# Kernel tuning notes

Measured on AMD Instinct MI355X. Metric: run time of the kernel, lower is better.

The kernel has to match this reference:

```python
import jax, jax.numpy as jnp
import numpy as np

K = 3            # CRF kernel size
THETA0 = 0.5     # color bandwidth
THETA1 = 30.0    # spatial bandwidth
ALPHA0 = 3.0     # kernel scale
BASE = 0.45      # label clamping base
CRF_ITERS = 10   # mean-field iterations
NMS_SIGMA = 2.0  # gaussian matrix-NMS sigma


def _unfold(x, k=K):
    # torch.nn.Unfold(k, stride=1, padding=k//2): (B, C, H, W) -> (B, C, k*k, H*W)
    B, C, H, W = x.shape
    p = k // 2
    xp = jnp.pad(x, ((0, 0), (0, 0), (p, p), (p, p)))
    patches = jnp.stack([xp[:, :, i:i + H, j:j + W]
                         for i in range(k) for j in range(k)], axis=2)
    return patches.reshape(B, C, k * k, H * W)


def _matrix_nms(seg_masks, cate_labels, cate_scores, sigma=NMS_SIGMA):
    n = seg_masks.shape[0]
    m = seg_masks.reshape(n, -1).astype(jnp.float32)
    sum_m = m.sum(axis=1)                         # (n,)
    inter = m @ m.T                               # (n, n)
    union = sum_m[None, :] + sum_m[:, None] - inter
    triu = jnp.triu(jnp.ones((n, n), dtype=bool), k=1)
    iou = jnp.where(triu, inter / union, 0.0)
    label_eq = (cate_labels[None, :] == cate_labels[:, None]) & triu
    decay_iou = jnp.where(label_eq, iou, 0.0)
    comp = decay_iou.max(axis=0)                  # compensate IoU per candidate
    decay = jnp.exp(-sigma * decay_iou ** 2)
    compm = jnp.exp(-sigma * comp ** 2)[:, None]  # broadcast over columns (torch expand+T)
    coef = (decay / compm).min(axis=0)
    return cate_scores * coef


def _crf(feature_map, x, targets):
    B, C, H, W = feature_map.shape
    k2 = K * K
    # gaussian pairwise kernel from (shifted) color features
    fm = feature_map + 10.0
    uf = _unfold(fm)                              # (B, C, k2, H*W)
    idx = np.arange(k2)
    spatial = ((idx // K - K // 2) ** 2 + (idx % K - K // 2) ** 2).astype(np.float32)
    color = -((uf - fm.reshape(B, C, 1, H * W)) ** 2).sum(axis=1) / (2.0 * THETA0 ** 2)
    kernel = ALPHA0 * jnp.exp(color - jnp.asarray(spatial)[None, :, None] / (2.0 * THETA1 ** 2))
    kernel = kernel[:, None]                      # (B, 1, k2, H*W)

    # unary init
    xt = x * targets
    xt = (xt > 0.5).astype(jnp.float32) * (1.0 - 2.0 * BASE) + BASE
    ret = jnp.concatenate([1.0 - xt, xt], axis=1)  # (B, 2, H, W)
    ones_t = jnp.ones_like(targets)
    for _ in range(CRF_ITERS):
        uf_x = _unfold(-jnp.log(ret.reshape(2 * B, 1, H, W))).reshape(B, 2, k2, H * W)
        aggre = (uf_x * kernel).sum(axis=2)        # (B, 2, H*W)
        f = jnp.exp(-aggre).reshape(B, 2, H, W)
        f = f * jnp.concatenate([ones_t, targets], axis=1)  # gate fg channel by targets
        f = f + 1e-6
        f = f / f.sum(axis=1, keepdims=True)
        ret = (f > 0.5).astype(jnp.float32) * (1.0 - 2.0 * BASE) + BASE
    masks = (ret[:, 1:] > 0.5).astype(jnp.float32)  # (B, 1, H, W)
    count = masks.reshape(B, -1).sum(axis=1)
    valid = ((count >= H * W * 0.05) & (count <= H * W * 0.95)).astype(jnp.float32)
    return masks, valid


def setup_inputs() -> dict:
    key = jax.random.key(0)
    k1, k2, k3, k4, k5, k6 = jax.random.split(key, 6)
    n, h, w = 256, 128, 128
    ni, c = 64, 3
    seg_masks = (jax.random.uniform(k1, (n, h, w)) > 0.5).astype(jnp.float32)
    cate_scores = jnp.sort(jax.random.uniform(k2, (n,)))[::-1]
    feature_map = jax.random.uniform(k3, (ni, c, h, w))
    x = jax.random.uniform(k4, (ni, 1, h, w))
    targets = (jax.random.uniform(k5, (ni, 1, h, w)) > 0.3).astype(jnp.float32)
    cate_labels = jax.random.randint(k6, (n,), 0, 80, dtype=jnp.int64)
    return {"seg_masks": seg_masks, "cate_scores": cate_scores,
            "feature_map": feature_map, "x": x, "targets": targets,
            "cate_labels": cate_labels}


def reference(seg_masks, cate_scores, feature_map, x, targets, cate_labels):
    scores = _matrix_nms(seg_masks, cate_labels, cate_scores)
    masks, valid = _crf(feature_map, x, targets)
    return scores, masks, valid
```

## Files before the change

kernel.cpp:

```cpp
#include <hip/hip_runtime.h>
#include <stdint.h>

#define HW 16384
#define NI 64
#define NM 256
#define WORDS 256

#define PR 136
#define TROWS 32
#define WROWS 52
#define NTHREADS 832
#define NBLK 256
#define SR 34
#define SPR 27
#define SPSZ (SPR * PR)

#define OFF_PACKED (2u << 20)
#define OFF_DIOUT  0x280000u
#define OFF_COMPM  0x2C0000u
#define OFF_CNT    0x2C1000u

__device__ __forceinline__ unsigned long long spread4(unsigned long long t) {
    t &= 0xFFFFull;
    t = (t | (t << 24)) & 0x000000FF000000FFull;
    t = (t | (t << 12)) & 0x000F000F000F000Full;
    t = (t | (t << 6))  & 0x0303030303030303ull;
    t = (t | (t << 3))  & 0x1111111111111111ull;
    return t;
}

__device__ __forceinline__ void load_row(const float* __restrict__ fb,
                                         const int y, const int xc,
                                         float (&u)[3][4]) {
    #pragma clang fp contract(off)
    if ((unsigned)y < 128u) {
        const int pp = y * 128 + xc;
        float4 v0 = *(const float4*)&fb[pp];
        float4 v1 = *(const float4*)&fb[HW + pp];
        float4 v2 = *(const float4*)&fb[2 * HW + pp];
        u[0][0]=v0.x+10.0f; u[0][1]=v0.y+10.0f; u[0][2]=v0.z+10.0f; u[0][3]=v0.w+10.0f;
        u[1][0]=v1.x+10.0f; u[1][1]=v1.y+10.0f; u[1][2]=v1.z+10.0f; u[1][3]=v1.w+10.0f;
        u[2][0]=v2.x+10.0f; u[2][1]=v2.y+10.0f; u[2][2]=v2.z+10.0f; u[2][3]=v2.w+10.0f;
    } else {
        #pragma unroll
        for (int c = 0; c < 3; ++c)
            #pragma unroll
            for (int j = 0; j < 4; ++j) u[c][j] = 0.0f;
    }
}

__device__ __forceinline__ float cell_res(float n0, float n1, float n2,
                                          float c0, float c1, float c2,
                                          float sp) {
    #pragma clang fp contract(off)
    float d0 = n0 - c0, d1 = n1 - c1, d2 = n2 - c2;
    float ss = d0 * d0;
    ss = ss + d1 * d1;
    ss = ss + d2 * d2;
    float color = (-ss) / 0.5f;
    return 3.0f * expf(color - sp);
}

__device__ __forceinline__ void compute_row(
    const float (&uc)[3][4], const float (&ut)[3][4],
    const float (&lt)[3], const float (&rt)[3], const float (&lc)[3],
    const bool in_y, const bool in_t, const int q, float4 (&out)[4]) {
    #pragma clang fp contract(off)
    const float sp1 = 1.0f / 1800.0f;
    const float sp2 = 2.0f / 1800.0f;
    float r[4];
    r[0] = r[1] = r[2] = r[3] = 0.0f;
    if (in_y && in_t) {
        if (q > 0)
            r[0] = cell_res(lt[0], lt[1], lt[2], uc[0][0], uc[1][0], uc[2][0], sp2);
        r[1] = cell_res(ut[0][0], ut[1][0], ut[2][0], uc[0][1], uc[1][1], uc[2][1], sp2);
        r[2] = cell_res(ut[0][1], ut[1][1], ut[2][1], uc[0][2], uc[1][2], uc[2][2], sp2);
        r[3] = cell_res(ut[0][2], ut[1][2], ut[2][2], uc[0][3], uc[1][3], uc[2][3], sp2);
    }
    out[0] = make_float4(r[0], r[1], r[2], r[3]);
    r[0] = r[1] = r[2] = r[3] = 0.0f;
    if (in_y && in_t) {
        r[0] = cell_res(ut[0][0], ut[1][0], ut[2][0], uc[0][0], uc[1][0], uc[2][0], sp1);
        r[1] = cell_res(ut[0][1], ut[1][1], ut[2][1], uc[0][1], uc[1][1], uc[2][1], sp1);
        r[2] = cell_res(ut[0][2], ut[1][2], ut[2][2], uc[0][2], uc[1][2], uc[2][2], sp1);
        r[3] = cell_res(ut[0][3], ut[1][3], ut[2][3], uc[0][3], uc[1][3], uc[2][3], sp1);
    }
    out[1] = make_float4(r[0], r[1], r[2], r[3]);
    r[0] = r[1] = r[2] = r[3] = 0.0f;
    if (in_y && in_t) {
        r[0] = cell_res(ut[0][1], ut[1][1], ut[2][1], uc[0][0], uc[1][0], uc[2][0], sp2);
        r[1] = cell_res(ut[0][2], ut[1][2], ut[2][2], uc[0][1], uc[1][1], uc[2][1], sp2);
        r[2] = cell_res(ut[0][3], ut[1][3], ut[2][3], uc[0][2], uc[1][2], uc[2][2], sp2);
        if (q < 31)
            r[3] = cell_res(rt[0], rt[1], rt[2], uc[0][3], uc[1][3], uc[2][3], sp2);
    }
    out[2] = make_float4(r[0], r[1], r[2], r[3]);
    r[0] = r[1] = r[2] = r[3] = 0.0f;
    if (in_y) {
        if (q > 0)
            r[0] = cell_res(lc[0], lc[1], lc[2], uc[0][0], uc[1][0], uc[2][0], sp1);
        r[1] = cell_res(uc[0][0], uc[1][0], uc[2][0], uc[0][1], uc[1][1], uc[2][1], sp1);
        r[2] = cell_res(uc[0][1], uc[1][1], uc[2][1], uc[0][2], uc[1][2], uc[2][2], sp1);
        r[3] = cell_res(uc[0][2], uc[1][2], uc[2][2], uc[0][3], uc[1][3], uc[2][3], sp1);
    }
    out[3] = make_float4(r[0], r[1], r[2], r[3]);
}

__device__ __forceinline__ void stage_init_row(
    const float* __restrict__ x, const float* __restrict__ targets,
    uint32_t* __restrict__ stw0, uint32_t* __restrict__ stw1, const int img,
    const int y, const int wrow, const int q, const int xc, const bool inimg) {
    #pragma clang fp contract(off)
    uint32_t st = 0;
    if (inimg) {
        const size_t gp = (size_t)img * HW + y * 128 + xc;
        const float4 xv = *(const float4*)(x + gp);
        const float4 tv = *(const float4*)(targets + gp);
        float xs[4] = {xv.x, xv.y, xv.z, xv.w};
        float ts[4] = {tv.x, tv.y, tv.z, tv.w};
        #pragma unroll
        for (int j = 0; j < 4; ++j) {
            float xt = xs[j] * ts[j];
            int b1 = (xt > 0.5f) ? 1 : 0;
            int tb = (ts[j] > 0.5f) ? 1 : 0;
            st |= (uint32_t)(b1 | ((b1 ^ 1) << 1) | (tb << 2)) << (8 * j);
        }
    }
    stw0[wrow * SR + 1 + q] = st;
    if (!inimg) stw1[wrow * SR + 1 + q] = 0;
    if (q == 0)  { stw0[wrow * SR + 0]  = 0; stw1[wrow * SR + 0]  = 0; }
    if (q == 31) { stw0[wrow * SR + 33] = 0; stw1[wrow * SR + 33] = 0; }
}

__device__ __forceinline__ uint32_t crf_core(const float (&kw)[9][4],
                                             const uint32_t (&in9)[9]) {
    #pragma clang fp contract(off)
    const float l45 = 0.7985076962177716f;
    const float l55 = 0.5978370007556204f;
    const uint32_t wcen = in9[4];
    float lx1r[3][6], lx0r[3][6];
    #pragma unroll
    for (int r = 0; r < 3; ++r) {
        const uint32_t wm = in9[r * 3 + 0];
        const uint32_t wc = in9[r * 3 + 1];
        const uint32_t wp = in9[r * 3 + 2];
        unsigned char b[6];
        b[0] = wm >> 24;
        b[1] = wc & 0xff; b[2] = (wc >> 8) & 0xff;
        b[3] = (wc >> 16) & 0xff; b[4] = wc >> 24;
        b[5] = wp & 0xff;
        #pragma unroll
        for (int m = 0; m < 6; ++m) {
            lx1r[r][m] = (b[m] & 1) ? l55 : l45;
            lx0r[r][m] = (b[m] & 2) ? l55 : l45;
        }
    }
    float a0[4] = {0.f, 0.f, 0.f, 0.f}, a1[4] = {0.f, 0.f, 0.f, 0.f};
    #pragma unroll
    for (int k = 0; k < 9; ++k) {
        const int r = k / 3, m0 = k % 3;
        #pragma unroll
        for (int j = 0; j < 4; ++j) {
            const float kwv = kw[k][j];
            const float t1 = lx1r[r][j + m0] * kwv;
            const float t0 = lx0r[r][j + m0] * kwv;
            a1[j] = a1[j] + t1;
            a0[j] = a0[j] + t0;
        }
    }
    uint32_t ow = 0;
    #pragma unroll
    for (int j = 0; j < 4; ++j) {
        const unsigned char sc = (wcen >> (8 * j)) & 0xffu;
        const float tval = (sc & 4) ? 1.0f : 0.0f;
        const float e1 = expf(-a1[j]);
        const float e0 = expf(-a0[j]);
        const float m1 = e1 * tval;
        const float f1 = m1 + 1e-6f;
        const float f0 = e0 + 1e-6f;
        const float den = f0 + f1;
        const float r1 = f1 / den;
        const float r0v = f0 / den;
        const int s1 = (r1 > 0.5f) ? 1 : 0;
        const int s0 = (r0v > 0.5f) ? 1 : 0;
        ow |= (uint32_t)(s1 | (s0 << 1) | (sc & 4)) << (8 * j);
    }
    return ow;
}

__global__ __launch_bounds__(832, 4) void crf10_kernel(
    const float* __restrict__ feat, const float* __restrict__ seg,
    unsigned long long* __restrict__ packed, const float* __restrict__ x,
    const float* __restrict__ targets, float* __restrict__ out,
    int* __restrict__ counters) {
    #pragma clang fp contract(off)
    __shared__ float strip[3 * SPSZ];
    __shared__ uint32_t stw0[WROWS * SR];
    __shared__ uint32_t stw1[WROWS * SR];
    __shared__ int chg[10];

    const int tid = threadIdx.x, bid = blockIdx.x;
    const int img = bid >> 2;
    const int r0 = (bid & 3) * TROWS;
    const int relp = tid >> 5;
    const int q = tid & 31;
    const int xc = q * 4;
    const int wrowA = 2 * relp, wrowB = wrowA + 1;
    const int yA = r0 - 10 + wrowA, yB = yA + 1;
    const bool inA = (unsigned)yA < 128u, inB = (unsigned)yB < 128u;
    const int sbaseA = wrowA * SR + 1 + q, sbaseB = wrowB * SR + 1 + q;
    const float* fb = feat + (size_t)img * 3 * HW;

    {
        const int wave = tid >> 6, lane = tid & 63;
        const int gw = bid * 13 + wave;
        for (int gwi = gw; gwi < 16384; gwi += 3328) {
            const int i = gwi >> 6, w4 = gwi & 63;
            const float4 v =
                *(const float4*)&seg[(size_t)i * HW + w4 * 256 + lane * 4];
            unsigned long long b0 = __ballot(v.x > 0.5f);
            unsigned long long b1 = __ballot(v.y > 0.5f);
            unsigned long long b2 = __ballot(v.z > 0.5f);
            unsigned long long b3 = __ballot(v.w > 0.5f);
            if (lane < 4) {
                const int sh = lane * 16;
                unsigned long long word = spread4(b0 >> sh)
                                        | (spread4(b1 >> sh) << 1)
                                        | (spread4(b2 >> sh) << 2)
                                        | (spread4(b3 >> sh) << 3);
                packed[(size_t)(w4 * 4 + lane) * NM + i] = word;
            }
        }
    }

    float uT[3][4], uA[3][4], uB[3][4];
    load_row(fb, yA - 1, xc, uT);
    load_row(fb, yA, xc, uA);
    float lT[3], rT[3], lA[3], rA[3], lB[3];
    #pragma unroll
    for (int c = 0; c < 3; ++c) {
        lT[c] = __shfl_up(uT[c][3], 1);
        rT[c] = __shfl_down(uT[c][0], 1);
        lA[c] = __shfl_up(uA[c][3], 1);
        rA[c] = __shfl_down(uA[c][0], 1);
    }
    float4 ap[4], bp[4];
    compute_row(uA, uT, lT, rT, lA, inA, (unsigned)(yA - 1) < 128u, q, ap);
    load_row(fb, yB, xc, uB);
    #pragma unroll
    for (int c = 0; c < 3; ++c) lB[c] = __shfl_up(uB[c][3], 1);
    compute_row(uB, uA, lA, rA, lB, inB, inA, q, bp);

    #pragma unroll
    for (int k = 0; k < 3; ++k) {
        *(float4*)&strip[k * SPSZ + relp * PR + 4 + xc] = ap[k];
        if (q == 0)
            *(float4*)&strip[k * SPSZ + relp * PR + 0] = make_float4(0, 0, 0, 0);
        if (q == 31)
            *(float4*)&strip[k * SPSZ + relp * PR + 132] = make_float4(0, 0, 0, 0);
    }
    stage_init_row(x, targets, stw0, stw1, img, yA, wrowA, q, xc, inA);
    stage_init_row(x, targets, stw0, stw1, img, yB, wrowB, q, xc, inB);
    if (tid < 10) chg[tid] = 0;

    float a_s5 = __shfl_down(ap[3].x, 1); if (q == 31) a_s5 = 0.0f;
    float b_s5 = __shfl_down(bp[3].x, 1); if (q == 31) b_s5 = 0.0f;
    float b_s6 = __shfl_up(bp[2].w, 1);   if (q == 0)  b_s6 = 0.0f;
    float b_s8 = __shfl_down(bp[0].x, 1); if (q == 31) b_s8 = 0.0f;
    __syncthreads();

    const float kwA[9][4] = {
        {ap[0].x, ap[0].y, ap[0].z, ap[0].w},
        {ap[1].x, ap[1].y, ap[1].z, ap[1].w},
        {ap[2].x, ap[2].y, ap[2].z, ap[2].w},
        {ap[3].x, ap[3].y, ap[3].z, ap[3].w},
        {3.0f, 3.0f, 3.0f, 3.0f},
        {ap[3].y, ap[3].z, ap[3].w, a_s5},
        {b_s6, bp[2].x, bp[2].y, bp[2].z},
        {bp[1].x, bp[1].y, bp[1].z, bp[1].w},
        {bp[0].y, bp[0].z, bp[0].w, b_s8}};

    uint32_t pinA[9], pinB[9];
    uint32_t powvA = 0, powvB = 0;
    bool hpA = false, hpB = false;
    int cur = 0;
    for (int s = 0; s < 10; ++s) {
        const int lo = (r0 - 9 + s < 0) ? 0 : r0 - 9 + s;
        const int hi = (r0 + 41 - s > 128) ? 128 : r0 + 41 - s;
        const bool actA = (yA >= lo) && (yA < hi);
        const bool actB = (yB >= lo) && (yB < hi);
        const uint32_t* sw = cur ? stw1 : stw0;
        uint32_t* swn = cur ? stw0 : stw1;
        bool changed = false;
        if (actA || actB) {
            const uint32_t ra0 = sw[sbaseA - 1], ra1 = sw[sbaseA], ra2 = sw[sbaseA + 1];
            const uint32_t rb0 = sw[sbaseB - 1], rb1 = sw[sbaseB], rb2 = sw[sbaseB + 1];
            if (actA) {
                const uint32_t in9[9] = {sw[sbaseA - SR - 1], sw[sbaseA - SR],
                                         sw[sbaseA - SR + 1], ra0, ra1, ra2,
                                         rb0, rb1, rb2};
                bool same = hpA;
                #pragma unroll
                for (int m = 0; m < 9; ++m) same = same && (in9[m] == pinA[m]);
                uint32_t ow;
                if (same) {
                    ow = powvA;
                } else {
                    ow = crf_core(kwA, in9);
                    #pragma unroll
                    for (int m = 0; m < 9; ++m) pinA[m] = in9[m];
                    powvA = ow;
                    hpA = true;
                }
                swn[sbaseA] = ow;
                changed = (ow != ra1);
            }
            if (actB) {
                const uint32_t in9[9] = {ra0, ra1, ra2, rb0, rb1, rb2,
                                         sw[sbaseB + SR - 1], sw[sbaseB + SR],
                                         sw[sbaseB + SR + 1]};
                bool same = hpB;
                #pragma unroll
                for (int m = 0; m < 9; ++m) same = same && (in9[m] == pinB[m]);
                uint32_t ow;
                if (same) {
                    ow = powvB;
                } else {
                    const int cb = (relp + 1) * PR + 4 + xc;
                    const float4 c_p0 = *(const float4*)&strip[0 * SPSZ + cb];
                    const float4 c_p1 = *(const float4*)&strip[1 * SPSZ + cb];
                    const float4 c_p2 = *(const float4*)&strip[2 * SPSZ + cb];
                    const float  c_s6 = strip[2 * SPSZ + cb - 1];
                    const float  c_s8 = strip[0 * SPSZ + cb + 4];
                    const float kwB[9][4] = {
                        {bp[0].x, bp[0].y, bp[0].z, bp[0].w},
                        {bp[1].x, bp[1].y, bp[1].z, bp[1].w},
                        {bp[2].x, bp[2].y, bp[2].z, bp[2].w},
                        {bp[3].x, bp[3].y, bp[3].z, bp[3].w},
                        {3.0f, 3.0f, 3.0f, 3.0f},
                        {bp[3].y, bp[3].z, bp[3].w, b_s5},
                        {c_s6, c_p2.x, c_p2.y, c_p2.z},
                        {c_p1.x, c_p1.y, c_p1.z, c_p1.w},
                        {c_p0.y, c_p0.z, c_p0.w, c_s8}};
                    ow = crf_core(kwB, in9);
                    #pragma unroll
                    for (int m = 0; m < 9; ++m) pinB[m] = in9[m];
                    powvB = ow;
                    hpB = true;
                }
                swn[sbaseB] = ow;
                changed = changed || (ow != rb1);
            }
        }
        unsigned long long bal = __ballot(changed);
        if ((tid & 63) == 0 && bal) atomicOr(&chg[s], 1);
        __syncthreads();
        if (chg[s] == 0) break;
        cur ^= 1;
    }

    int cnt = 0;
    {
        const uint32_t* swf = cur ? stw1 : stw0;
        float* om = out + NM + (size_t)img * HW;
        if (yA >= r0 && yA < r0 + TROWS) {
            const uint32_t w = swf[sbaseA];
            *(float4*)(om + yA * 128 + xc) =
                make_float4((float)(w & 1), (float)((w >> 8) & 1),
                            (float)((w >> 16) & 1), (float)((w >> 24) & 1));
            cnt += __popc(w & 0x01010101u);
        }
        if (yB >= r0 && yB < r0 + TROWS) {
            const uint32_t w = swf[sbaseB];
            *(float4*)(om + yB * 128 + xc) =
                make_float4((float)(w & 1), (float)((w >> 8) & 1),
                            (float)((w >> 16) & 1), (float)((w >> 24) & 1));
            cnt += __popc(w & 0x01010101u);
        }
    }
    __syncthreads();
    {
        int* cred = (int*)strip;
        cred[tid] = cnt;
        if (tid < 192) cred[832 + tid] = 0;
        __syncthreads();
        for (int off = 512; off > 0; off >>= 1) {
            if (tid < off) cred[tid] += cred[tid + off];
            __syncthreads();
        }
        if (tid == 0) counters[bid] = cred[0];
    }
}

__global__ __launch_bounds__(256) void diou_compm_kernel(
    const unsigned long long* __restrict__ packed, const int* __restrict__ labels,
    float* __restrict__ diouT, float* __restrict__ compm) {
    #pragma clang fp contract(off)
    __shared__ unsigned long long colj[WORDS];
    __shared__ float red[NM];
    const int j = blockIdx.x, i = threadIdx.x;
    colj[i] = packed[i * NM + j];
    __syncthreads();
    int inter = 0, si = 0, sj = 0;
    for (int w = 0; w < WORDS; ++w) {
        unsigned long long a = colj[w];
        unsigned long long b = packed[w * NM + i];
        inter += __popcll(a & b);
        sj += __popcll(a);
        si += __popcll(b);
    }
    float d = 0.0f;
    if (j > i && labels[i] == labels[j]) {
        float u = (float)(si + sj - inter);
        d = (float)inter / u;
    }
    diouT[j * NM + i] = d;
    red[i] = d;
    __syncthreads();
    for (int off = 128; off > 0; off >>= 1) {
        if (i < off) red[i] = fmaxf(red[i], red[i + off]);
        __syncthreads();
    }
    if (i == 0) {
        float m = red[0];
        float t = m * m;
        compm[j] = expf(-2.0f * t);
    }
}

__global__ __launch_bounds__(256) void coef_valid_kernel(
    const float* __restrict__ scores, const float* __restrict__ diouT,
    const float* __restrict__ compm, const int* __restrict__ counters,
    float* __restrict__ out) {
    #pragma clang fp contract(off)
    __shared__ float red[NM];
    const int bid = blockIdx.x, tid = threadIdx.x;
    float d = diouT[bid * NM + tid];
    float dd = d * d;
    float dec = expf(-2.0f * dd);
    red[tid] = dec / compm[tid];
    __syncthreads();
    for (int off = 128; off > 0; off >>= 1) {
        if (tid < off) red[tid] = fminf(red[tid], red[tid + off]);
        __syncthreads();
    }
    if (tid == 0) out[bid] = scores[bid] * red[0];
    if (bid == 0 && tid < NI) {
        int c = counters[4 * tid] + counters[4 * tid + 1] +
                counters[4 * tid + 2] + counters[4 * tid + 3];
        out[NM + (size_t)NI * HW + tid] = (c >= 820 && c <= 15564) ? 1.0f : 0.0f;
    }
}

extern "C" void kernel_launch(void* const* d_in, const int* in_sizes, int n_in,
                              void* d_out, int out_size, void* d_ws, size_t ws_size,
                              hipStream_t stream) {
    const float* seg = (const float*)d_in[0];
    const float* cate_scores = (const float*)d_in[1];
    const float* feat = (const float*)d_in[2];
    const float* x = (const float*)d_in[3];
    const float* targets = (const float*)d_in[4];
    const int* labels = (const int*)d_in[5];
    float* out = (float*)d_out;
    char* ws = (char*)d_ws;

    unsigned long long* packed = (unsigned long long*)(ws + OFF_PACKED);
    float* diouT = (float*)(ws + OFF_DIOUT);
    float* compm = (float*)(ws + OFF_COMPM);
    int* counters = (int*)(ws + OFF_CNT);

    crf10_kernel<<<NBLK, NTHREADS, 0, stream>>>(feat, seg, packed, x, targets,
                                                out, counters);
    diou_compm_kernel<<<NM, 256, 0, stream>>>(packed, labels, diouT, compm);
    coef_valid_kernel<<<NM, 256, 0, stream>>>(cate_scores, diouT, compm,
                                              counters, out);
}
```

Baseline: 161.2 us.

## Split diou word loop across 1024 threads and hoist CRF global loads earlier

```diff
diff --git a/kernel.cpp b/kernel.cpp
--- a/kernel.cpp
+++ b/kernel.cpp
@@ -106,16 +106,12 @@
     out[3] = make_float4(r[0], r[1], r[2], r[3]);
 }
 
-__device__ __forceinline__ void stage_init_row(
-    const float* __restrict__ x, const float* __restrict__ targets,
-    uint32_t* __restrict__ stw0, uint32_t* __restrict__ stw1, const int img,
-    const int y, const int wrow, const int q, const int xc, const bool inimg) {
+__device__ __forceinline__ void stage_commit_row(
+    const float4 xv, const float4 tv, uint32_t* __restrict__ stw0,
+    uint32_t* __restrict__ stw1, const int wrow, const int q, const bool inimg) {
     #pragma clang fp contract(off)
     uint32_t st = 0;
     if (inimg) {
-        const size_t gp = (size_t)img * HW + y * 128 + xc;
-        const float4 xv = *(const float4*)(x + gp);
-        const float4 tv = *(const float4*)(targets + gp);
         float xs[4] = {xv.x, xv.y, xv.z, xv.w};
         float ts[4] = {tv.x, tv.y, tv.z, tv.w};
         #pragma unroll
@@ -210,6 +206,22 @@
     const bool inA = (unsigned)yA < 128u, inB = (unsigned)yB < 128u;
     const int sbaseA = wrowA * SR + 1 + q, sbaseB = wrowB * SR + 1 + q;
     const float* fb = feat + (size_t)img * 3 * HW;
+
+    float uT[3][4], uA[3][4], uB[3][4];
+    load_row(fb, yA - 1, xc, uT);
+    load_row(fb, yA, xc, uA);
+    load_row(fb, yB, xc, uB);
+    float4 xvA = make_float4(0, 0, 0, 0), tvA = xvA, xvB = xvA, tvB = xvA;
+    if (inA) {
+        const size_t gp = (size_t)img * HW + yA * 128 + xc;
+        xvA = *(const float4*)(x + gp);
+        tvA = *(const float4*)(targets + gp);
+    }
+    if (inB) {
+        const size_t gp = (size_t)img * HW + yB * 128 + xc;
+        xvB = *(const float4*)(x + gp);
+        tvB = *(const float4*)(targets + gp);
+    }
 
     {
         const int wave = tid >> 6, lane = tid & 63;
@@ -233,9 +245,6 @@
         }
     }
 
-    float uT[3][4], uA[3][4], uB[3][4];
-    load_row(fb, yA - 1, xc, uT);
-    load_row(fb, yA, xc, uA);
     float lT[3], rT[3], lA[3], rA[3], lB[3];
     #pragma unroll
     for (int c = 0; c < 3; ++c) {
@@ -243,12 +252,10 @@
         rT[c] = __shfl_down(uT[c][0], 1);
         lA[c] = __shfl_up(uA[c][3], 1);
         rA[c] = __shfl_down(uA[c][0], 1);
+        lB[c] = __shfl_up(uB[c][3], 1);
     }
     float4 ap[4], bp[4];
     compute_row(uA, uT, lT, rT, lA, inA, (unsigned)(yA - 1) < 128u, q, ap);
-    load_row(fb, yB, xc, uB);
-    #pragma unroll
-    for (int c = 0; c < 3; ++c) lB[c] = __shfl_up(uB[c][3], 1);
     compute_row(uB, uA, lA, rA, lB, inB, inA, q, bp);
 
     #pragma unroll
@@ -259,8 +266,8 @@
         if (q == 31)
             *(float4*)&strip[k * SPSZ + relp * PR + 132] = make_float4(0, 0, 0, 0);
     }
-    stage_init_row(x, targets, stw0, stw1, img, yA, wrowA, q, xc, inA);
-    stage_init_row(x, targets, stw0, stw1, img, yB, wrowB, q, xc, inB);
+    stage_commit_row(xvA, tvA, stw0, stw1, wrowA, q, inA);
+    stage_commit_row(xvB, tvB, stw0, stw1, wrowB, q, inB);
     if (tid < 10) chg[tid] = 0;
 
     float a_s5 = __shfl_down(ap[3].x, 1); if (q == 31) a_s5 = 0.0f;
@@ -392,36 +399,47 @@
     }
 }
 
-__global__ __launch_bounds__(256) void diou_compm_kernel(
+__global__ __launch_bounds__(1024) void diou_compm_kernel(
     const unsigned long long* __restrict__ packed, const int* __restrict__ labels,
     float* __restrict__ diouT, float* __restrict__ compm) {
     #pragma clang fp contract(off)
     __shared__ unsigned long long colj[WORDS];
+    __shared__ int pin[1024], psi[1024], psj[1024];
     __shared__ float red[NM];
-    const int j = blockIdx.x, i = threadIdx.x;
-    colj[i] = packed[i * NM + j];
+    const int j = blockIdx.x, tid = threadIdx.x;
+    const int i = tid & 255, wq = tid >> 8;
+    if (tid < NM) colj[tid] = packed[tid * NM + j];
     __syncthreads();
     int inter = 0, si = 0, sj = 0;
-    for (int w = 0; w < WORDS; ++w) {
+    const int w0 = wq * 64;
+    #pragma unroll 4
+    for (int w = w0; w < w0 + 64; ++w) {
         unsigned long long a = colj[w];
         unsigned long long b = packed[w * NM + i];
         inter += __popcll(a & b);
         sj += __popcll(a);
         si += __popcll(b);
     }
-    float d = 0.0f;
-    if (j > i && labels[i] == labels[j]) {
-        float u = (float)(si + sj - inter);
-        d = (float)inter / u;
-    }
-    diouT[j * NM + i] = d;
-    red[i] = d;
+    pin[tid] = inter; psi[tid] = si; psj[tid] = sj;
+    __syncthreads();
+    if (tid < NM) {
+        const int I = pin[tid] + pin[tid + 256] + pin[tid + 512] + pin[tid + 768];
+        const int S = psi[tid] + psi[tid + 256] + psi[tid + 512] + psi[tid + 768];
+        const int J = psj[tid] + psj[tid + 256] + psj[tid + 512] + psj[tid + 768];
+        float d = 0.0f;
+        if (j > tid && labels[tid] == labels[j]) {
+            float u = (float)(S + J - I);
+            d = (float)I / u;
+        }
+        diouT[j * NM + tid] = d;
+        red[tid] = d;
+    }
     __syncthreads();
     for (int off = 128; off > 0; off >>= 1) {
-        if (i < off) red[i] = fmaxf(red[i], red[i + off]);
+        if (tid < off) red[tid] = fmaxf(red[tid], red[tid + off]);
         __syncthreads();
     }
-    if (i == 0) {
+    if (tid == 0) {
         float m = red[0];
         float t = m * m;
         compm[j] = expf(-2.0f * t);
@@ -471,7 +489,7 @@
 
     crf10_kernel<<<NBLK, NTHREADS, 0, stream>>>(feat, seg, packed, x, targets,
                                                 out, counters);
-    diou_compm_kernel<<<NM, 256, 0, stream>>>(packed, labels, diouT, compm);
+    diou_compm_kernel<<<NM, 1024, 0, stream>>>(packed, labels, diouT, compm);
     coef_valid_kernel<<<NM, 256, 0, stream>>>(cate_scores, diouT, compm,
                                               counters, out);
 }
```

Measured after the change: 163.3 us. About the same (+1.3%).
